# Kernel tuning notes

Hardware: AMD Instinct MI355X
Metric: run time of the kernel (lower is better)

The kernel has to match this reference:

```python
import jax, jax.numpy as jnp
import numpy as np
import math

B, L, D = 4, 4096, 64

def setup_inputs() -> dict:
    key = jax.random.key(0)
    kq, kk, kv = jax.random.split(key, 3)
    q = jax.random.normal(kq, (B, L, D), dtype=jnp.float32)
    k = jax.random.normal(kk, (B, L, D), dtype=jnp.float32)
    v = jax.random.normal(kv, (B, L, D), dtype=jnp.float32)
    return {"q": q, "k": k, "v": v}

def reference(q, k, v):
    d_model = k.shape[-1]
    # score[b,i,j] = <q_i, k_j> / sqrt(d)   -> [B, L, L]
    score = jnp.einsum('bid,bjd->bij', q, k) / math.sqrt(d_model)
    attn = jax.nn.softmax(score.astype(jnp.float32), axis=-1)
    # Faithful to source: output = (v^T @ attn)^T = attn^T @ v
    # output[b,j,d] = sum_i attn[b,i,j] * v[b,i,d]
    out = jnp.einsum('bij,bid->bjd', attn, v)
    return out
```

## Files before the change

kernel.cpp:

```cpp
#include <hip/hip_runtime.h>
#include <hip/hip_bf16.h>

#define LQ 4096
#define DD 64
#define NB 4
#define NTOT ((size_t)NB * LQ * DD)
#define NROW ((size_t)NB * LQ)

typedef __attribute__((ext_vector_type(4))) float f32x4;
typedef __attribute__((ext_vector_type(8))) short short8;
typedef __attribute__((ext_vector_type(2))) unsigned int uint2v;
typedef __attribute__((ext_vector_type(4))) unsigned short ushort4v;

static __device__ __forceinline__ unsigned short f2bf(float x) {
  __hip_bfloat16 h = __float2bfloat16(x);
  return __builtin_bit_cast(unsigned short, h);
}
static __device__ __forceinline__ float bf2f(unsigned short u) {
  unsigned int v = ((unsigned int)u) << 16;
  return __builtin_bit_cast(float, v);
}
static __device__ __forceinline__ float ex2(float x) { return __builtin_amdgcn_exp2f(x); }

static __device__ __forceinline__ void gl_lds16(const unsigned short* g, unsigned short* l) {
  __builtin_amdgcn_global_load_lds(
      (const __attribute__((address_space(1))) unsigned int*)g,
      (__attribute__((address_space(3))) unsigned int*)l, 16, 0, 0);
}

#define C1 0.18033688011112042f

__global__ __launch_bounds__(256) void prep_kernel(
    const float* __restrict__ q, const float* __restrict__ k,
    const float* __restrict__ v,
    unsigned short* __restrict__ Qb, unsigned short* __restrict__ Kb,
    unsigned short* __restrict__ Vb)
{
  const int arr = blockIdx.x >> 9;
  const size_t off = (((size_t)(blockIdx.x & 511)) * 256 + threadIdx.x) * 8;
  const float* s = arr == 0 ? q : arr == 1 ? k : v;
  unsigned short* d = arr == 0 ? Qb : arr == 1 ? Kb : Vb;
  const f32x4 x0 = *(const f32x4*)(s + off);
  const f32x4 x1 = *(const f32x4*)(s + off + 4);
  ushort4v o0 = { f2bf(x0[0]), f2bf(x0[1]), f2bf(x0[2]), f2bf(x0[3]) };
  ushort4v o1 = { f2bf(x1[0]), f2bf(x1[1]), f2bf(x1[2]), f2bf(x1[3]) };
  *(ushort4v*)(d + off) = o0;
  *(ushort4v*)(d + off + 4) = o1;
}

__global__ __launch_bounds__(256, 2) void stats_kernel(
    const unsigned short* __restrict__ Qb, const unsigned short* __restrict__ Kb,
    float* __restrict__ part_ls)
{
  __shared__ __align__(16) unsigned short stK[3][2048];
  const int bx = blockIdx.x;
  const int jc = bx & 7, it = (bx >> 3) & 15, b = bx >> 7;
  const int tid = threadIdx.x, w = tid >> 6, lane = tid & 63;
  const int l15 = lane & 15, g = lane >> 4;
  const int i0 = it * 256 + w * 64;
  const int jbase = jc * 512;
  const unsigned short* Kbase = Kb + (size_t)b * LQ * DD;

  short8 aq[4][2];
#pragma unroll
  for (int is = 0; is < 4; ++is)
#pragma unroll
    for (int kh = 0; kh < 2; ++kh)
      aq[is][kh] = *(const short8*)(Qb + ((size_t)b * LQ + i0 + is * 16 + l15) * DD + kh * 32 + g * 8);

  float ls[4][4];
#pragma unroll
  for (int is = 0; is < 4; ++is)
#pragma unroll
    for (int qq = 0; qq < 4; ++qq) ls[is][qq] = 0.f;

  const int srow = w * 8 + (lane >> 3);
  const int scol = ((lane & 7) ^ (lane >> 3)) << 3;

  gl_lds16(Kbase + (size_t)(jbase + srow) * DD + scol, &stK[0][w * 512]);
  gl_lds16(Kbase + (size_t)(jbase + 32 + srow) * DD + scol, &stK[1][w * 512]);
  asm volatile("s_waitcnt vmcnt(1)" ::: "memory");
  __builtin_amdgcn_s_barrier();

  for (int itr = 0; itr < 16; ++itr) {
    const int cur = itr % 3;
    const int tn = (itr + 2 < 16) ? itr + 2 : 15;
    gl_lds16(Kbase + (size_t)(jbase + tn * 32 + srow) * DD + scol, &stK[(itr + 2) % 3][w * 512]);

    short8 kf[2][2];
#pragma unroll
    for (int jsub = 0; jsub < 2; ++jsub)
#pragma unroll
      for (int kh = 0; kh < 2; ++kh) {
        const int row = jsub * 16 + l15;
        kf[jsub][kh] = *(const short8*)(&stK[cur][row * 64 + (((kh * 4 + g) ^ (l15 & 7)) << 3)]);
      }
#pragma unroll
    for (int is = 0; is < 4; ++is)
#pragma unroll
      for (int jsub = 0; jsub < 2; ++jsub) {
        f32x4 tt = __builtin_amdgcn_mfma_f32_16x16x32_bf16(
            aq[is][0], kf[jsub][0], (f32x4){0.f, 0.f, 0.f, 0.f}, 0, 0, 0);
        tt = __builtin_amdgcn_mfma_f32_16x16x32_bf16(aq[is][1], kf[jsub][1], tt, 0, 0, 0);
#pragma unroll
        for (int qq = 0; qq < 4; ++qq) ls[is][qq] += ex2(tt[qq] * C1);
      }
    asm volatile("s_waitcnt vmcnt(1)" ::: "memory");
    __builtin_amdgcn_s_barrier();
  }
#pragma unroll
  for (int mask = 1; mask <= 8; mask <<= 1)
#pragma unroll
    for (int is = 0; is < 4; ++is)
#pragma unroll
      for (int qq = 0; qq < 4; ++qq) ls[is][qq] += __shfl_xor(ls[is][qq], mask, 64);
  if (l15 == 0) {
#pragma unroll
    for (int is = 0; is < 4; ++is)
#pragma unroll
      for (int qq = 0; qq < 4; ++qq)
        part_ls[(size_t)jc * NROW + b * LQ + i0 + is * 16 + g * 4 + qq] = ls[is][qq];
  }
}

__global__ __launch_bounds__(256) void combine_kernel(
    const float* __restrict__ part_ls, const unsigned short* __restrict__ Vb,
    unsigned short* __restrict__ Vs)
{
  const size_t base = ((size_t)blockIdx.x * 256 + threadIdx.x) * 8;
  const int r = (int)(base >> 6);
  float l = 0.f;
#pragma unroll
  for (int jc = 0; jc < 8; ++jc) l += part_ls[(size_t)jc * NROW + r];
  const float s = 1.0f / l;
  const ushort4v a = *(const ushort4v*)(Vb + base);
  const ushort4v c = *(const ushort4v*)(Vb + base + 4);
  ushort4v oa = { f2bf(bf2f(a[0]) * s), f2bf(bf2f(a[1]) * s),
                  f2bf(bf2f(a[2]) * s), f2bf(bf2f(a[3]) * s) };
  ushort4v oc = { f2bf(bf2f(c[0]) * s), f2bf(bf2f(c[1]) * s),
                  f2bf(bf2f(c[2]) * s), f2bf(bf2f(c[3]) * s) };
  *(ushort4v*)(Vs + base) = oa;
  *(ushort4v*)(Vs + base + 4) = oc;
}

__global__ __launch_bounds__(512, 2) void attn_out_kernel(
    const unsigned short* __restrict__ Qb, const unsigned short* __restrict__ Kb,
    const unsigned short* __restrict__ Vs, float* __restrict__ out)
{
  __shared__ __align__(16) unsigned short stage[8][2][4096];
  __shared__ __align__(16) unsigned short Pall[8 * 1088];

  const int bx = blockIdx.x;
  const int jt = bx & 63;
  const int b  = bx >> 6;
  const int tid = threadIdx.x, w = tid >> 6, lane = tid & 63;
  const int l15 = lane & 15, g = lane >> 4;
  const int j0 = jt * 64;

  const unsigned short* Qbase = Qb + (size_t)b * LQ * DD;
  const unsigned short* Vbase = Vs + (size_t)b * LQ * DD;

  short8 ka[4][2];
#pragma unroll
  for (int js = 0; js < 4; ++js)
#pragma unroll
    for (int kh = 0; kh < 2; ++kh)
      ka[js][kh] = *(const short8*)(Kb + ((size_t)b * LQ + j0 + js * 16 + l15) * DD + kh * 32 + g * 8);

  f32x4 acc[4][4];
#pragma unroll
  for (int js = 0; js < 4; ++js)
#pragma unroll
    for (int ds = 0; ds < 4; ++ds) acc[js][ds] = (f32x4){0.f, 0.f, 0.f, 0.f};

  const int ibase = w * 512;
  const int qrow = lane >> 3;
  const int qcol = ((lane & 7) ^ (lane >> 3)) << 3;
  const int vrow = (lane >> 5) * 4 + ((lane >> 1) & 3);
  const int vcol = (((lane >> 3) & 3) << 4) + ((lane & 1) << 3);

  unsigned short* Pw = &Pall[w * 1088];
  const unsigned pbyte = (unsigned)(size_t)Pw;

#define STAGE(BUF, I0) do { \
    _Pragma("unroll") \
    for (int kk = 0; kk < 4; ++kk) { \
      gl_lds16(Qbase + (size_t)((I0) + kk * 8 + qrow) * DD + qcol, &stage[w][BUF][kk * 512]); \
      gl_lds16(Vbase + (size_t)((I0) + kk * 8 + vrow) * DD + vcol, &stage[w][BUF][2048 + kk * 512]); \
    } \
  } while (0)

  STAGE(0, ibase);

  for (int itr = 0; itr < 16; ++itr) {
    const int cur = itr & 1;
    const int tn = (itr + 1 < 16) ? itr + 1 : itr;
    STAGE(cur ^ 1, ibase + tn * 32);
    asm volatile("s_waitcnt vmcnt(8)" ::: "memory");

    const unsigned sbyte = (unsigned)(size_t)&stage[w][cur][0];

    short8 qf[2][2];
#pragma unroll
    for (int is = 0; is < 2; ++is)
#pragma unroll
      for (int kh = 0; kh < 2; ++kh) {
        const int row = is * 16 + l15;
        qf[is][kh] = *(const short8*)(&stage[w][cur][row * 64 + (((kh * 4 + g) ^ (l15 & 7)) << 3)]);
      }

    unsigned long long v0, v1, v2, v3, v4, v5, v6, v7;
    const unsigned av = sbyte + 4096 + g * 1024 + l15 * 8;
    asm volatile(
        "ds_read_b64_tr_b16 %0, %8\n\t"
        "ds_read_b64_tr_b16 %1, %8 offset:512\n\t"
        "ds_read_b64_tr_b16 %2, %8 offset:128\n\t"
        "ds_read_b64_tr_b16 %3, %8 offset:640\n\t"
        "ds_read_b64_tr_b16 %4, %8 offset:256\n\t"
        "ds_read_b64_tr_b16 %5, %8 offset:768\n\t"
        "ds_read_b64_tr_b16 %6, %8 offset:384\n\t"
        "ds_read_b64_tr_b16 %7, %8 offset:896\n\t"
        "s_waitcnt lgkmcnt(0)"
        : "=&v"(v0), "=&v"(v1), "=&v"(v2), "=&v"(v3),
          "=&v"(v4), "=&v"(v5), "=&v"(v6), "=&v"(v7)
        : "v"(av) : "memory");
    union U { unsigned long long u[2]; short8 s; };
    U vf0, vf1, vf2, vf3;
    vf0.u[0] = v0; vf0.u[1] = v1;
    vf1.u[0] = v2; vf1.u[1] = v3;
    vf2.u[0] = v4; vf2.u[1] = v5;
    vf3.u[0] = v6; vf3.u[1] = v7;

#pragma unroll
    for (int h = 0; h < 2; ++h) {
      __builtin_amdgcn_s_setprio(1);
#pragma unroll
      for (int jsl = 0; jsl < 2; ++jsl) {
        const int js = h * 2 + jsl;
#pragma unroll
        for (int is = 0; is < 2; ++is) {
          f32x4 tt = __builtin_amdgcn_mfma_f32_16x16x32_bf16(
              ka[js][0], qf[is][0], (f32x4){0.f, 0.f, 0.f, 0.f}, 0, 0, 0);
          tt = __builtin_amdgcn_mfma_f32_16x16x32_bf16(ka[js][1], qf[is][1], tt, 0, 0, 0);
          const unsigned a0 = __builtin_bit_cast(unsigned, ex2(tt[0] * C1)) + 0x8000u;
          const unsigned a1 = __builtin_bit_cast(unsigned, ex2(tt[1] * C1)) + 0x8000u;
          const unsigned a2 = __builtin_bit_cast(unsigned, ex2(tt[2] * C1)) + 0x8000u;
          const unsigned a3 = __builtin_bit_cast(unsigned, ex2(tt[3] * C1)) + 0x8000u;
          uint2v uu;
          uu[0] = __builtin_amdgcn_perm(a1, a0, 0x07060302u);
          uu[1] = __builtin_amdgcn_perm(a3, a2, 0x07060302u);
          const int il = is * 16 + l15;
          *(uint2v*)(&Pw[jsl * 544 + (il >> 2) * 68 + (il & 3) * 16 + g * 4]) = uu;
        }
      }
      __builtin_amdgcn_s_setprio(0);

      unsigned long long p0, p1, p2, p3;
      const unsigned ap = pbyte + g * 272 + l15 * 8;
      asm volatile(
          "s_waitcnt lgkmcnt(0)\n\t"
          "ds_read_b64_tr_b16 %0, %4\n\t"
          "ds_read_b64_tr_b16 %1, %4 offset:136\n\t"
          "ds_read_b64_tr_b16 %2, %4 offset:1088\n\t"
          "ds_read_b64_tr_b16 %3, %4 offset:1224\n\t"
          "s_waitcnt lgkmcnt(0)"
          : "=&v"(p0), "=&v"(p1), "=&v"(p2), "=&v"(p3)
          : "v"(ap) : "memory");
      U pa0, pa1;
      pa0.u[0] = p0; pa0.u[1] = p1;
      pa1.u[0] = p2; pa1.u[1] = p3;
      __builtin_amdgcn_s_setprio(1);
      acc[h*2+0][0] = __builtin_amdgcn_mfma_f32_16x16x32_bf16(pa0.s, vf0.s, acc[h*2+0][0], 0, 0, 0);
      acc[h*2+0][1] = __builtin_amdgcn_mfma_f32_16x16x32_bf16(pa0.s, vf1.s, acc[h*2+0][1], 0, 0, 0);
      acc[h*2+0][2] = __builtin_amdgcn_mfma_f32_16x16x32_bf16(pa0.s, vf2.s, acc[h*2+0][2], 0, 0, 0);
      acc[h*2+0][3] = __builtin_amdgcn_mfma_f32_16x16x32_bf16(pa0.s, vf3.s, acc[h*2+0][3], 0, 0, 0);
      acc[h*2+1][0] = __builtin_amdgcn_mfma_f32_16x16x32_bf16(pa1.s, vf0.s, acc[h*2+1][0], 0, 0, 0);
      acc[h*2+1][1] = __builtin_amdgcn_mfma_f32_16x16x32_bf16(pa1.s, vf1.s, acc[h*2+1][1], 0, 0, 0);
      acc[h*2+1][2] = __builtin_amdgcn_mfma_f32_16x16x32_bf16(pa1.s, vf2.s, acc[h*2+1][2], 0, 0, 0);
      acc[h*2+1][3] = __builtin_amdgcn_mfma_f32_16x16x32_bf16(pa1.s, vf3.s, acc[h*2+1][3], 0, 0, 0);
      __builtin_amdgcn_s_setprio(0);
    }
  }
#undef STAGE

  asm volatile("s_waitcnt vmcnt(0)" ::: "memory");
  __syncthreads();
  float* red = (float*)&stage[0][0][0];
#pragma unroll
  for (int js = 0; js < 4; ++js)
#pragma unroll
    for (int ds = 0; ds < 4; ++ds)
#pragma unroll
      for (int qq = 0; qq < 4; ++qq)
        red[w * 4096 + (js * 16 + g * 4 + qq) * 64 + ds * 16 + l15] = acc[js][ds][qq];
  __syncthreads();
  {
    const int lr = lane >> 4;
    const int d0 = (lane & 15) * 4;
    float* op = out + ((size_t)b * LQ + j0 + w * 8) * DD;
#pragma unroll
    for (int rr = 0; rr < 2; ++rr) {
      const int row = rr * 4 + lr;
      f32x4 s = (f32x4){0.f, 0.f, 0.f, 0.f};
#pragma unroll
      for (int u = 0; u < 8; ++u) {
        const f32x4 t = *(const f32x4*)&red[u * 4096 + (w * 8 + row) * 64 + d0];
        s[0] += t[0]; s[1] += t[1]; s[2] += t[2]; s[3] += t[3];
      }
      *(f32x4*)(op + row * 64 + d0) = s;
    }
  }
}

extern "C" void kernel_launch(void* const* d_in, const int* in_sizes, int n_in,
                              void* d_out, int out_size, void* d_ws, size_t ws_size,
                              hipStream_t stream) {
  const float* q = (const float*)d_in[0];
  const float* k = (const float*)d_in[1];
  const float* v = (const float*)d_in[2];

  unsigned short* Qb = (unsigned short*)d_ws;
  unsigned short* Kb = Qb + NTOT;
  unsigned short* Vb = Kb + NTOT;
  unsigned short* Vs = Vb + NTOT;
  float* part_ls = (float*)(Vs + NTOT);
  float* outp = (float*)d_out;

  prep_kernel<<<1536, 256, 0, stream>>>(q, k, v, Qb, Kb, Vb);
  stats_kernel<<<NB * 16 * 8, 256, 0, stream>>>(Qb, Kb, part_ls);
  combine_kernel<<<512, 256, 0, stream>>>(part_ls, Vb, Vs);
  attn_out_kernel<<<NB * 64, 512, 0, stream>>>(Qb, Kb, Vs, outp);
}
```

Baseline: 58.23 us.

## Share Q/V staging across wave pairs and split stats over more j-chunks

In attn_out_kernel, waves now work in pairs: one wave stages Q and the other stages V into a shared LDS buffer. Each wave covers 32 output columns over 1024 rows instead of 64 columns over 512 rows. This halves per-block staging LDS and the global loads issued per wave, at the cost of a full-block barrier and a vmcnt(0) wait every iteration, which reduces load/compute overlap. Separately, stats_kernel is split into 16 key chunks instead of 8, which doubles the grid for better latency hiding, and combine_kernel now sums 16 partials.

```diff
diff --git a/kernel.cpp b/kernel.cpp
--- a/kernel.cpp
+++ b/kernel.cpp
@@ -48,17 +48,17 @@
   *(ushort4v*)(d + off + 4) = o1;
 }
 
-__global__ __launch_bounds__(256, 2) void stats_kernel(
+__global__ __launch_bounds__(256, 4) void stats_kernel(
     const unsigned short* __restrict__ Qb, const unsigned short* __restrict__ Kb,
     float* __restrict__ part_ls)
 {
   __shared__ __align__(16) unsigned short stK[3][2048];
   const int bx = blockIdx.x;
-  const int jc = bx & 7, it = (bx >> 3) & 15, b = bx >> 7;
+  const int jc = bx & 15, it = (bx >> 4) & 15, b = bx >> 8;
   const int tid = threadIdx.x, w = tid >> 6, lane = tid & 63;
   const int l15 = lane & 15, g = lane >> 4;
   const int i0 = it * 256 + w * 64;
-  const int jbase = jc * 512;
+  const int jbase = jc * 256;
   const unsigned short* Kbase = Kb + (size_t)b * LQ * DD;
 
   short8 aq[4][2];
@@ -82,9 +82,9 @@
   asm volatile("s_waitcnt vmcnt(1)" ::: "memory");
   __builtin_amdgcn_s_barrier();
 
-  for (int itr = 0; itr < 16; ++itr) {
+  for (int itr = 0; itr < 8; ++itr) {
     const int cur = itr % 3;
-    const int tn = (itr + 2 < 16) ? itr + 2 : 15;
+    const int tn = (itr + 2 < 8) ? itr + 2 : 7;
     gl_lds16(Kbase + (size_t)(jbase + tn * 32 + srow) * DD + scol, &stK[(itr + 2) % 3][w * 512]);
 
     short8 kf[2][2];
@@ -131,7 +131,7 @@
   const int r = (int)(base >> 6);
   float l = 0.f;
 #pragma unroll
-  for (int jc = 0; jc < 8; ++jc) l += part_ls[(size_t)jc * NROW + r];
+  for (int jc = 0; jc < 16; ++jc) l += part_ls[(size_t)jc * NROW + r];
   const float s = 1.0f / l;
   const ushort4v a = *(const ushort4v*)(Vb + base);
   const ushort4v c = *(const ushort4v*)(Vb + base + 4);
@@ -143,62 +143,67 @@
   *(ushort4v*)(Vs + base + 4) = oc;
 }
 
-__global__ __launch_bounds__(512, 2) void attn_out_kernel(
+__global__ __launch_bounds__(512, 4) void attn_out_kernel(
     const unsigned short* __restrict__ Qb, const unsigned short* __restrict__ Kb,
     const unsigned short* __restrict__ Vs, float* __restrict__ out)
 {
-  __shared__ __align__(16) unsigned short stage[8][2][4096];
-  __shared__ __align__(16) unsigned short Pall[8 * 1088];
+  __shared__ __align__(16) unsigned short stage[4][2][4096];
+  __shared__ __align__(16) unsigned short Pall[8 * 1024];
 
   const int bx = blockIdx.x;
   const int jt = bx & 63;
   const int b  = bx >> 6;
   const int tid = threadIdx.x, w = tid >> 6, lane = tid & 63;
+  const int p = w >> 1, sub = w & 1;
   const int l15 = lane & 15, g = lane >> 4;
-  const int j0 = jt * 64;
+  const int j0 = jt * 64 + sub * 32;
 
   const unsigned short* Qbase = Qb + (size_t)b * LQ * DD;
   const unsigned short* Vbase = Vs + (size_t)b * LQ * DD;
 
-  short8 ka[4][2];
-#pragma unroll
-  for (int js = 0; js < 4; ++js)
+  short8 ka[2][2];
+#pragma unroll
+  for (int jsl = 0; jsl < 2; ++jsl)
 #pragma unroll
     for (int kh = 0; kh < 2; ++kh)
-      ka[js][kh] = *(const short8*)(Kb + ((size_t)b * LQ + j0 + js * 16 + l15) * DD + kh * 32 + g * 8);
-
-  f32x4 acc[4][4];
-#pragma unroll
-  for (int js = 0; js < 4; ++js)
-#pragma unroll
-    for (int ds = 0; ds < 4; ++ds) acc[js][ds] = (f32x4){0.f, 0.f, 0.f, 0.f};
-
-  const int ibase = w * 512;
+      ka[jsl][kh] = *(const short8*)(Kb + ((size_t)b * LQ + j0 + jsl * 16 + l15) * DD + kh * 32 + g * 8);
+
+  f32x4 acc[2][4];
+#pragma unroll
+  for (int jsl = 0; jsl < 2; ++jsl)
+#pragma unroll
+    for (int ds = 0; ds < 4; ++ds) acc[jsl][ds] = (f32x4){0.f, 0.f, 0.f, 0.f};
+
+  const int ibase = p * 1024;
   const int qrow = lane >> 3;
   const int qcol = ((lane & 7) ^ (lane >> 3)) << 3;
   const int vrow = (lane >> 5) * 4 + ((lane >> 1) & 3);
   const int vcol = (((lane >> 3) & 3) << 4) + ((lane & 1) << 3);
 
-  unsigned short* Pw = &Pall[w * 1088];
+  unsigned short* Pw = &Pall[w * 1024];
   const unsigned pbyte = (unsigned)(size_t)Pw;
 
 #define STAGE(BUF, I0) do { \
-    _Pragma("unroll") \
-    for (int kk = 0; kk < 4; ++kk) { \
-      gl_lds16(Qbase + (size_t)((I0) + kk * 8 + qrow) * DD + qcol, &stage[w][BUF][kk * 512]); \
-      gl_lds16(Vbase + (size_t)((I0) + kk * 8 + vrow) * DD + vcol, &stage[w][BUF][2048 + kk * 512]); \
+    if (sub == 0) { \
+      _Pragma("unroll") \
+      for (int kk = 0; kk < 4; ++kk) \
+        gl_lds16(Qbase + (size_t)((I0) + kk * 8 + qrow) * DD + qcol, &stage[p][BUF][kk * 512]); \
+    } else { \
+      _Pragma("unroll") \
+      for (int kk = 0; kk < 4; ++kk) \
+        gl_lds16(Vbase + (size_t)((I0) + kk * 8 + vrow) * DD + vcol, &stage[p][BUF][2048 + kk * 512]); \
     } \
   } while (0)
 
   STAGE(0, ibase);
 
-  for (int itr = 0; itr < 16; ++itr) {
+  for (int itr = 0; itr < 32; ++itr) {
     const int cur = itr & 1;
-    const int tn = (itr + 1 < 16) ? itr + 1 : itr;
-    STAGE(cur ^ 1, ibase + tn * 32);
-    asm volatile("s_waitcnt vmcnt(8)" ::: "memory");
-
-    const unsigned sbyte = (unsigned)(size_t)&stage[w][cur][0];
+    asm volatile("s_waitcnt vmcnt(0)" ::: "memory");
+    __builtin_amdgcn_s_barrier();
+    if (itr + 1 < 32) STAGE(cur ^ 1, ibase + (itr + 1) * 32);
+
+    const unsigned sbyte = (unsigned)(size_t)&stage[p][cur][0];
 
     short8 qf[2][2];
 #pragma unroll
@@ -206,7 +211,7 @@
 #pragma unroll
       for (int kh = 0; kh < 2; ++kh) {
         const int row = is * 16 + l15;
-        qf[is][kh] = *(const short8*)(&stage[w][cur][row * 64 + (((kh * 4 + g) ^ (l15 & 7)) << 3)]);
+        qf[is][kh] = *(const short8*)(&stage[p][cur][row * 64 + (((kh * 4 + g) ^ (l15 & 7)) << 3)]);
       }
 
     unsigned long long v0, v1, v2, v3, v4, v5, v6, v7;
@@ -231,55 +236,51 @@
     vf2.u[0] = v4; vf2.u[1] = v5;
     vf3.u[0] = v6; vf3.u[1] = v7;
 
-#pragma unroll
-    for (int h = 0; h < 2; ++h) {
-      __builtin_amdgcn_s_setprio(1);
-#pragma unroll
-      for (int jsl = 0; jsl < 2; ++jsl) {
-        const int js = h * 2 + jsl;
-#pragma unroll
-        for (int is = 0; is < 2; ++is) {
-          f32x4 tt = __builtin_amdgcn_mfma_f32_16x16x32_bf16(
-              ka[js][0], qf[is][0], (f32x4){0.f, 0.f, 0.f, 0.f}, 0, 0, 0);
-          tt = __builtin_amdgcn_mfma_f32_16x16x32_bf16(ka[js][1], qf[is][1], tt, 0, 0, 0);
-          const unsigned a0 = __builtin_bit_cast(unsigned, ex2(tt[0] * C1)) + 0x8000u;
-          const unsigned a1 = __builtin_bit_cast(unsigned, ex2(tt[1] * C1)) + 0x8000u;
-          const unsigned a2 = __builtin_bit_cast(unsigned, ex2(tt[2] * C1)) + 0x8000u;
-          const unsigned a3 = __builtin_bit_cast(unsigned, ex2(tt[3] * C1)) + 0x8000u;
-          uint2v uu;
-          uu[0] = __builtin_amdgcn_perm(a1, a0, 0x07060302u);
-          uu[1] = __builtin_amdgcn_perm(a3, a2, 0x07060302u);
-          const int il = is * 16 + l15;
-          *(uint2v*)(&Pw[jsl * 544 + (il >> 2) * 68 + (il & 3) * 16 + g * 4]) = uu;
-        }
-      }
-      __builtin_amdgcn_s_setprio(0);
-
-      unsigned long long p0, p1, p2, p3;
-      const unsigned ap = pbyte + g * 272 + l15 * 8;
-      asm volatile(
-          "s_waitcnt lgkmcnt(0)\n\t"
-          "ds_read_b64_tr_b16 %0, %4\n\t"
-          "ds_read_b64_tr_b16 %1, %4 offset:136\n\t"
-          "ds_read_b64_tr_b16 %2, %4 offset:1088\n\t"
-          "ds_read_b64_tr_b16 %3, %4 offset:1224\n\t"
-          "s_waitcnt lgkmcnt(0)"
-          : "=&v"(p0), "=&v"(p1), "=&v"(p2), "=&v"(p3)
-          : "v"(ap) : "memory");
-      U pa0, pa1;
-      pa0.u[0] = p0; pa0.u[1] = p1;
-      pa1.u[0] = p2; pa1.u[1] = p3;
-      __builtin_amdgcn_s_setprio(1);
-      acc[h*2+0][0] = __builtin_amdgcn_mfma_f32_16x16x32_bf16(pa0.s, vf0.s, acc[h*2+0][0], 0, 0, 0);
-      acc[h*2+0][1] = __builtin_amdgcn_mfma_f32_16x16x32_bf16(pa0.s, vf1.s, acc[h*2+0][1], 0, 0, 0);
-      acc[h*2+0][2] = __builtin_amdgcn_mfma_f32_16x16x32_bf16(pa0.s, vf2.s, acc[h*2+0][2], 0, 0, 0);
-      acc[h*2+0][3] = __builtin_amdgcn_mfma_f32_16x16x32_bf16(pa0.s, vf3.s, acc[h*2+0][3], 0, 0, 0);
-      acc[h*2+1][0] = __builtin_amdgcn_mfma_f32_16x16x32_bf16(pa1.s, vf0.s, acc[h*2+1][0], 0, 0, 0);
-      acc[h*2+1][1] = __builtin_amdgcn_mfma_f32_16x16x32_bf16(pa1.s, vf1.s, acc[h*2+1][1], 0, 0, 0);
-      acc[h*2+1][2] = __builtin_amdgcn_mfma_f32_16x16x32_bf16(pa1.s, vf2.s, acc[h*2+1][2], 0, 0, 0);
-      acc[h*2+1][3] = __builtin_amdgcn_mfma_f32_16x16x32_bf16(pa1.s, vf3.s, acc[h*2+1][3], 0, 0, 0);
-      __builtin_amdgcn_s_setprio(0);
+    __builtin_amdgcn_s_setprio(1);
+#pragma unroll
+    for (int jsl = 0; jsl < 2; ++jsl) {
+#pragma unroll
+      for (int is = 0; is < 2; ++is) {
+        f32x4 tt = __builtin_amdgcn_mfma_f32_16x16x32_bf16(
+            ka[jsl][0], qf[is][0], (f32x4){0.f, 0.f, 0.f, 0.f}, 0, 0, 0);
+        tt = __builtin_amdgcn_mfma_f32_16x16x32_bf16(ka[jsl][1], qf[is][1], tt, 0, 0, 0);
+        const unsigned a0 = __builtin_bit_cast(unsigned, ex2(tt[0] * C1)) + 0x8000u;
+        const unsigned a1 = __builtin_bit_cast(unsigned, ex2(tt[1] * C1)) + 0x8000u;
+        const unsigned a2 = __builtin_bit_cast(unsigned, ex2(tt[2] * C1)) + 0x8000u;
+        const unsigned a3 = __builtin_bit_cast(unsigned, ex2(tt[3] * C1)) + 0x8000u;
+        uint2v uu;
+        uu[0] = __builtin_amdgcn_perm(a1, a0, 0x07060302u);
+        uu[1] = __builtin_amdgcn_perm(a3, a2, 0x07060302u);
+        const int il = is * 16 + l15;
+        *(uint2v*)(&Pw[jsl * 512 + (il >> 2) * 64 + (il & 3) * 16 + g * 4]) = uu;
+      }
     }
+    __builtin_amdgcn_s_setprio(0);
+
+    unsigned long long p0, p1, p2, p3;
+    const unsigned ap = pbyte + g * 256 + l15 * 8;
+    asm volatile(
+        "s_waitcnt lgkmcnt(0)\n\t"
+        "ds_read_b64_tr_b16 %0, %4\n\t"
+        "ds_read_b64_tr_b16 %1, %4 offset:128\n\t"
+        "ds_read_b64_tr_b16 %2, %4 offset:1024\n\t"
+        "ds_read_b64_tr_b16 %3, %4 offset:1152\n\t"
+        "s_waitcnt lgkmcnt(0)"
+        : "=&v"(p0), "=&v"(p1), "=&v"(p2), "=&v"(p3)
+        : "v"(ap) : "memory");
+    U pa0, pa1;
+    pa0.u[0] = p0; pa0.u[1] = p1;
+    pa1.u[0] = p2; pa1.u[1] = p3;
+    __builtin_amdgcn_s_setprio(1);
+    acc[0][0] = __builtin_amdgcn_mfma_f32_16x16x32_bf16(pa0.s, vf0.s, acc[0][0], 0, 0, 0);
+    acc[0][1] = __builtin_amdgcn_mfma_f32_16x16x32_bf16(pa0.s, vf1.s, acc[0][1], 0, 0, 0);
+    acc[0][2] = __builtin_amdgcn_mfma_f32_16x16x32_bf16(pa0.s, vf2.s, acc[0][2], 0, 0, 0);
+    acc[0][3] = __builtin_amdgcn_mfma_f32_16x16x32_bf16(pa0.s, vf3.s, acc[0][3], 0, 0, 0);
+    acc[1][0] = __builtin_amdgcn_mfma_f32_16x16x32_bf16(pa1.s, vf0.s, acc[1][0], 0, 0, 0);
+    acc[1][1] = __builtin_amdgcn_mfma_f32_16x16x32_bf16(pa1.s, vf1.s, acc[1][1], 0, 0, 0);
+    acc[1][2] = __builtin_amdgcn_mfma_f32_16x16x32_bf16(pa1.s, vf2.s, acc[1][2], 0, 0, 0);
+    acc[1][3] = __builtin_amdgcn_mfma_f32_16x16x32_bf16(pa1.s, vf3.s, acc[1][3], 0, 0, 0);
+    __builtin_amdgcn_s_setprio(0);
   }
 #undef STAGE
 
@@ -287,27 +288,27 @@
   __syncthreads();
   float* red = (float*)&stage[0][0][0];
 #pragma unroll
-  for (int js = 0; js < 4; ++js)
+  for (int jsl = 0; jsl < 2; ++jsl)
 #pragma unroll
     for (int ds = 0; ds < 4; ++ds)
 #pragma unroll
       for (int qq = 0; qq < 4; ++qq)
-        red[w * 4096 + (js * 16 + g * 4 + qq) * 64 + ds * 16 + l15] = acc[js][ds][qq];
+        red[w * 2048 + (jsl * 16 + g * 4 + qq) * 64 + ds * 16 + l15] = acc[jsl][ds][qq];
   __syncthreads();
   {
     const int lr = lane >> 4;
     const int d0 = (lane & 15) * 4;
-    float* op = out + ((size_t)b * LQ + j0 + w * 8) * DD;
+    float* op = out + ((size_t)b * LQ + jt * 64 + sub * 32) * DD;
 #pragma unroll
     for (int rr = 0; rr < 2; ++rr) {
-      const int row = rr * 4 + lr;
+      const int jj = p * 8 + rr * 4 + lr;
       f32x4 s = (f32x4){0.f, 0.f, 0.f, 0.f};
 #pragma unroll
-      for (int u = 0; u < 8; ++u) {
-        const f32x4 t = *(const f32x4*)&red[u * 4096 + (w * 8 + row) * 64 + d0];
+      for (int u = 0; u < 4; ++u) {
+        const f32x4 t = *(const f32x4*)&red[(u * 2 + sub) * 2048 + jj * 64 + d0];
         s[0] += t[0]; s[1] += t[1]; s[2] += t[2]; s[3] += t[3];
       }
-      *(f32x4*)(op + row * 64 + d0) = s;
+      *(f32x4*)(op + jj * 64 + d0) = s;
     }
   }
 }
@@ -327,7 +328,7 @@
   float* outp = (float*)d_out;
 
   prep_kernel<<<1536, 256, 0, stream>>>(q, k, v, Qb, Kb, Vb);
-  stats_kernel<<<NB * 16 * 8, 256, 0, stream>>>(Qb, Kb, part_ls);
+  stats_kernel<<<NB * 16 * 16, 256, 0, stream>>>(Qb, Kb, part_ls);
   combine_kernel<<<512, 256, 0, stream>>>(part_ls, Vb, Vs);
   attn_out_kernel<<<NB * 64, 512, 0, stream>>>(Qb, Kb, Vs, outp);
 }
```

Measured after the change: 92.81 us. +59.4%, slower.
